# Optimization experiments

Measured on AMD Instinct MI355X. Metric: run time of the kernel, lower is better.

## Reference

```python
import jax, jax.numpy as jnp
import numpy as np

B_SZ, SEQ, D_MODEL = 2, 4096, 2048
EXPAND, D_STATE, D_CONV = 2, 16, 4
D_INNER = EXPAND * D_MODEL          # 4096
DT_RANK = -(-D_MODEL // 16)         # 128


def setup_inputs() -> dict:
    key = jax.random.key(0)
    ks = jax.random.split(key, 9)
    s = 0.02
    hidden_states = jax.random.normal(ks[0], (B_SZ, SEQ, D_MODEL), jnp.float32)
    W_in = jax.random.normal(ks[1], (2 * D_INNER, D_MODEL), jnp.float32) * s
    conv_w = jax.random.normal(ks[2], (D_INNER, D_CONV), jnp.float32) * 0.2
    conv_b = jnp.zeros((D_INNER,), jnp.float32)
    W_x = jax.random.normal(ks[3], (DT_RANK + 2 * D_STATE, D_INNER), jnp.float32) * s
    W_dt = jax.random.normal(ks[4], (D_INNER, DT_RANK), jnp.float32) * (DT_RANK ** -0.5)
    # dt bias so softplus(dt) ~ [1e-3, 0.1] as in Mamba init
    u = jax.random.uniform(ks[5], (D_INNER,), jnp.float32)
    dt = jnp.exp(u * (np.log(0.1) - np.log(1e-3)) + np.log(1e-3))
    dt_bias = dt + jnp.log(-jnp.expm1(-dt))  # inverse softplus
    # S4D-real init: A = -[1..d_state] per channel (kept negative for stability)
    A = -jnp.tile(jnp.arange(1.0, D_STATE + 1.0, dtype=jnp.float32), (D_INNER, 1))
    D = jnp.ones((D_INNER,), jnp.float32)
    W_out = jax.random.normal(ks[6], (D_MODEL, D_INNER), jnp.float32) * s
    return {"hidden_states": hidden_states, "W_in": W_in, "conv_w": conv_w,
            "conv_b": conv_b, "W_x": W_x, "W_dt": W_dt, "dt_bias": dt_bias,
            "A": A, "D": D, "W_out": W_out}


def _mamba_fwd(hidden_states, W_in, conv_w, conv_b, W_x, W_dt, dt_bias, A, D, W_out):
    # in_proj -> (B, L, 2*d_inner); split into x and gate z
    xz = jnp.einsum('bld,ed->ble', hidden_states, W_in)
    x, z = jnp.split(xz, 2, axis=-1)                    # (B,L,d_inner) each
    # causal depthwise conv1d over L (kernel d_conv), then SiLU
    d_conv = conv_w.shape[1]
    xp = jnp.pad(x, ((0, 0), (d_conv - 1, 0), (0, 0)))
    L = x.shape[1]
    xc = conv_b
    acc = jnp.zeros_like(x)
    for k in range(d_conv):                             # small fixed loop (4 taps)
        acc = acc + xp[:, k:k + L, :] * conv_w[:, k]
    x = jax.nn.silu(acc + conv_b)
    # x_proj -> dt_rank + 2*d_state
    ssm = jnp.einsum('bld,ed->ble', x, W_x)
    dt_r, Bm, Cm = jnp.split(ssm, [DT_RANK, DT_RANK + D_STATE], axis=-1)
    delta = jax.nn.softplus(jnp.einsum('blr,dr->bld', dt_r, W_dt) + dt_bias)
    # selective scan: h_t = exp(delta_t*A) h_{t-1} + delta_t*B_t*u_t ; y_t = C_t.h_t
    def step(state, inp):
        d_t, u_t, B_t, C_t = inp                        # (B,Di),(B,Di),(B,N),(B,N)
        dA = jnp.exp(d_t[..., None] * A)                # (B,Di,N)
        state = state * dA + (d_t * u_t)[..., None] * B_t[:, None, :]
        y = jnp.einsum('bdn,bn->bd', state, C_t)
        return state, y
    init = jnp.zeros((x.shape[0], D_INNER, D_STATE), jnp.float32)
    xs = (jnp.swapaxes(delta, 0, 1), jnp.swapaxes(x, 0, 1),
          jnp.swapaxes(Bm, 0, 1), jnp.swapaxes(Cm, 0, 1))
    _, ys = jax.lax.scan(step, init, xs)
    y = jnp.swapaxes(ys, 0, 1) + x * D                  # D skip connection
    y = y * jax.nn.silu(z)                              # gate
    return jnp.einsum('bld,md->blm', y, W_out)


def reference(hidden_states, W_in, conv_w, conv_b, W_x, W_dt, dt_bias, A, D, W_out):
    return _mamba_fwd(hidden_states, W_in, conv_w, conv_b, W_x, W_dt,
                      dt_bias, A, D, W_out)
```

## Files before the change

kernel.cpp:

```cpp
#include <hip/hip_runtime.h>
#include <hip/hip_bf16.h>
#include <cstdint>
#include <cstddef>

typedef _Float16 f16x8 __attribute__((ext_vector_type(8)));
typedef _Float16 f16x4 __attribute__((ext_vector_type(4)));
typedef float    f32x4 __attribute__((ext_vector_type(4)));

#define AS1 __attribute__((address_space(1)))
#define AS3 __attribute__((address_space(3)))

static constexpr int B_SZ = 2, SEQ = 4096, D_MODEL = 2048;
static constexpr int D_INNER = 4096, D_STATE = 16, D_CONV = 4, DT_RANK = 128;
static constexpr int M_ROWS = B_SZ * SEQ;
static constexpr int SSM_W  = DT_RANK + 2 * D_STATE;

__global__ __launch_bounds__(256) void k_cvt_f16(const float* __restrict__ in,
                                                 _Float16* __restrict__ out, int n4) {
    int i = blockIdx.x * 256 + threadIdx.x;
    if (i >= n4) return;
    f32x4 v = ((const f32x4*)in)[i];
    f16x4 h;
    h[0] = (_Float16)v[0]; h[1] = (_Float16)v[1];
    h[2] = (_Float16)v[2]; h[3] = (_Float16)v[3];
    ((f16x4*)out)[i] = h;
}

__global__ __launch_bounds__(256) void k_extract_dtr(const float* __restrict__ ssm,
                                                     _Float16* __restrict__ dtr) {
    int idx = blockIdx.x * 256 + threadIdx.x;
    if (idx >= M_ROWS * (DT_RANK / 4)) return;
    int m  = idx >> 5;
    int j4 = (idx & 31) * 4;
    f32x4 v = *(const f32x4*)&ssm[(size_t)m * SSM_W + j4];
    f16x4 h;
    h[0] = (_Float16)v[0]; h[1] = (_Float16)v[1];
    h[2] = (_Float16)v[2]; h[3] = (_Float16)v[3];
    *(f16x4*)&dtr[(size_t)m * DT_RANK + j4] = h;
}

template <int EPI>
__global__ __launch_bounds__(512, 2) void k_gemm256(
    const _Float16* __restrict__ A, const _Float16* __restrict__ Bm, int K, int nbx,
    void* __restrict__ out0, void* __restrict__ out1, int ldc) {
    __shared__ _Float16 lA[4][256][32];
    __shared__ _Float16 lB[4][256][32];

    const int tid  = threadIdx.x;
    const int l    = tid & 63;
    const int w    = tid >> 6;
    const int fr   = l & 15, fq = l >> 4;
    const int wrA  = (w >> 2) * 128;
    const int wcB  = (w & 3) * 64;

    const int nwg = gridDim.x;
    const int qq  = nwg >> 3;
    const int id  = (blockIdx.x & 7) * qq + (blockIdx.x >> 3);
    const int bx  = id % nbx, by = id / nbx;
    const int tileM = by * 256, tileN = bx * 256;

    const int srow = (l >> 2);
    const int cofs = (((l & 3) ^ ((l >> 2) & 3)) << 3);
    const int cswz = ((fq ^ (fr & 3)) << 3);

    f32x4 acc[8][4];
#pragma unroll
    for (int m = 0; m < 8; m++)
#pragma unroll
        for (int n = 0; n < 4; n++) acc[m][n] = (f32x4)0.f;

    const int NK = K >> 5;

    auto stage = [&](int ss, int kk) {
#pragma unroll
        for (int i = 0; i < 2; ++i) {
            const int u   = w * 2 + i;
            const int row = u * 16 + srow;
            const _Float16* ga = A  + (size_t)(tileM + row) * K + kk + cofs;
            const _Float16* gb = Bm + (size_t)(tileN + row) * K + kk + cofs;
            __builtin_amdgcn_global_load_lds((const AS1 void*)ga, (AS3 void*)&lA[ss][u * 16][0], 16, 0, 0);
            __builtin_amdgcn_global_load_lds((const AS1 void*)gb, (AS3 void*)&lB[ss][u * 16][0], 16, 0, 0);
        }
    };

    auto compute = [&](int ss) {
        f16x8 af[8], bf[4];
#pragma unroll
        for (int m = 0; m < 8; ++m)
            af[m] = *(const f16x8*)&lA[ss][wrA + m * 16 + fr][cswz];
#pragma unroll
        for (int n = 0; n < 4; ++n)
            bf[n] = *(const f16x8*)&lB[ss][wcB + n * 16 + fr][cswz];
        __builtin_amdgcn_s_setprio(1);
#pragma unroll
        for (int m = 0; m < 8; ++m)
#pragma unroll
            for (int n = 0; n < 4; ++n)
                acc[m][n] = __builtin_amdgcn_mfma_f32_16x16x32_f16(af[m], bf[n], acc[m][n], 0, 0, 0);
        __builtin_amdgcn_s_setprio(0);
    };

    stage(0, 0); stage(1, 32); stage(2, 64);
    asm volatile("s_waitcnt vmcnt(8)" ::: "memory");
    __builtin_amdgcn_s_barrier();

    for (int s = 0; s < NK - 3; ++s) {
        stage((s + 3) & 3, (s + 3) << 5);
        compute(s & 3);
        asm volatile("s_waitcnt vmcnt(8)" ::: "memory");
        __builtin_amdgcn_s_barrier();
    }
    compute((NK - 3) & 3);
    asm volatile("s_waitcnt vmcnt(4)" ::: "memory");
    __builtin_amdgcn_s_barrier();
    compute((NK - 2) & 3);
    asm volatile("s_waitcnt vmcnt(0)" ::: "memory");
    __builtin_amdgcn_s_barrier();
    compute((NK - 1) & 3);

#pragma unroll
    for (int m = 0; m < 8; ++m) {
#pragma unroll
        for (int n = 0; n < 4; ++n) {
            const int r0 = tileM + wrA + m * 16 + fq * 4;
            const int c  = tileN + wcB + n * 16 + fr;
#pragma unroll
            for (int q = 0; q < 4; ++q) {
                const float  v  = acc[m][n][q];
                const size_t mm = (size_t)(r0 + q);
                if (EPI == 0) {
                    if (c < D_INNER)
                        ((_Float16*)out0)[mm * D_INNER + c] = (_Float16)v;
                    else
                        ((_Float16*)out1)[mm * D_INNER + (c - D_INNER)] = (_Float16)v;
                } else {
                    ((float*)out0)[mm * ldc + c] = v;
                }
            }
        }
    }
}

template <int BM, int BN, int EPI>
__global__ __launch_bounds__(256) void k_gemm_nt(
    const _Float16* __restrict__ A, const _Float16* __restrict__ Bm, int K,
    int lda, int ldb, void* __restrict__ out0,
    const float* __restrict__ bias, int ldc) {
    __shared__ _Float16 a_lds[BM][32];
    __shared__ _Float16 b_lds[BN][32];
    constexpr int MR = BM / 32;
    constexpr int NR = BN / 32;
    const int tid  = threadIdx.x;
    const int lane = tid & 63;
    const int wid  = tid >> 6;
    const int wr = wid >> 1, wc = wid & 1;
    const int tileM = blockIdx.y * BM;
    const int tileN = blockIdx.x * BN;

    f32x4 acc[MR][NR];
    for (int i = 0; i < MR; i++)
        for (int j = 0; j < NR; j++) acc[i][j] = (f32x4)0.f;

    constexpr int IS_A = BM / 16;
    constexpr int IS_B = BN / 16;
    const int srow = lane >> 2;
    const int skof = (lane & 3) * 8;
    const int fr = lane & 15, fq = lane >> 4;

    for (int kk = 0; kk < K; kk += 32) {
        if (kk) __syncthreads();
        for (int is = wid; is < IS_A + IS_B; is += 4) {
            const bool isA = is < IS_A;
            const int  li  = isA ? is : is - IS_A;
            const int  row = li * 16 + srow;
            const _Float16* g =
                isA ? (A  + (size_t)(tileM + row) * lda + kk + skof)
                    : (Bm + (size_t)(tileN + row) * ldb + kk + skof);
            char* lp = ((char*)(isA ? &a_lds[0][0] : &b_lds[0][0])) + (size_t)li * 1024;
            __builtin_amdgcn_global_load_lds((const AS1 void*)g, (AS3 void*)lp, 16, 0, 0);
        }
        __syncthreads();

        f16x8 af[MR], bf[NR];
#pragma unroll
        for (int i = 0; i < MR; i++)
            af[i] = *(const f16x8*)&a_lds[wr * (BM / 2) + i * 16 + fr][fq * 8];
#pragma unroll
        for (int j = 0; j < NR; j++)
            bf[j] = *(const f16x8*)&b_lds[wc * (BN / 2) + j * 16 + fr][fq * 8];
#pragma unroll
        for (int i = 0; i < MR; i++)
#pragma unroll
            for (int j = 0; j < NR; j++)
                acc[i][j] = __builtin_amdgcn_mfma_f32_16x16x32_f16(af[i], bf[j], acc[i][j], 0, 0, 0);
    }

#pragma unroll
    for (int i = 0; i < MR; i++) {
#pragma unroll
        for (int j = 0; j < NR; j++) {
            const int r0 = tileM + wr * (BM / 2) + i * 16 + fq * 4;
            const int c  = tileN + wc * (BN / 2) + j * 16 + fr;
#pragma unroll
            for (int q = 0; q < 4; q++) {
                const float  v = acc[i][j][q];
                const size_t m = (size_t)(r0 + q);
                if (EPI == 1) {
                    ((float*)out0)[m * ldc + c] = v;
                } else {
                    float x  = v + bias[c];
                    float sp = (x > 20.f) ? x : log1pf(__expf(x));
                    ((_Float16*)out0)[m * ldc + c] = (_Float16)sp;
                }
            }
        }
    }
}

__global__ __launch_bounds__(256) void k_conv_silu(const _Float16* __restrict__ x,
                                                   const float* __restrict__ w,
                                                   const float* __restrict__ bias,
                                                   _Float16* __restrict__ out) {
    const int idx = blockIdx.x * 256 + threadIdx.x;
    const int d4 = idx & (D_INNER / 4 - 1);
    const int t  = (idx >> 10) & (SEQ - 1);
    const int b  = idx >> 22;
    const int d  = d4 * 4;
    const size_t rowbase = (size_t)b * SEQ * D_INNER;

    f32x4 wv[4];
#pragma unroll
    for (int i = 0; i < 4; i++) wv[i] = ((const f32x4*)w)[d + i];

    float acc[4];
#pragma unroll
    for (int i = 0; i < 4; i++) acc[i] = bias[d + i];
#pragma unroll
    for (int k = 0; k < D_CONV; k++) {
        int ti = t - (D_CONV - 1) + k;
        if (ti < 0) continue;
        f16x4 xv = *(const f16x4*)&x[rowbase + (size_t)ti * D_INNER + d];
#pragma unroll
        for (int i = 0; i < 4; i++) acc[i] += (float)xv[i] * wv[i][k];
    }
    f16x4 o;
#pragma unroll
    for (int i = 0; i < 4; i++) {
        float v = acc[i];
        o[i] = (_Float16)(v / (1.f + __expf(-v)));
    }
    *(f16x4*)&out[rowbase + (size_t)t * D_INNER + d] = o;
}

template <int CH, typename ST>
__global__ __launch_bounds__(256) void k_scan_p1(const _Float16* __restrict__ delta_h,
                                                 const _Float16* __restrict__ xc,
                                                 const float* __restrict__ ssm,
                                                 const float* __restrict__ Aptr,
                                                 ST* __restrict__ Sbuf,
                                                 ST* __restrict__ Pbuf) {
    constexpr int NCH = SEQ / CH;
    constexpr float L2E = 1.44269504088896f;
    const int bid   = blockIdx.x;
    const int dg    = bid & 15;
    const int chunk = (bid >> 4) % NCH;
    const int b     = bid / (16 * NCH);
    const int d     = dg * 256 + threadIdx.x;

    __shared__ float bsh[CH][D_STATE];
    const size_t rb = (size_t)b * SEQ + (size_t)chunk * CH;
    for (int i = threadIdx.x; i < CH * D_STATE; i += 256) {
        int t = i >> 4, n = i & 15;
        bsh[t][n] = ssm[(rb + t) * SSM_W + DT_RANK + n];
    }
    __syncthreads();

    float a2[D_STATE];
#pragma unroll
    for (int n = 0; n < D_STATE; n++) a2[n] = Aptr[(size_t)d * D_STATE + n] * L2E;
    float st[D_STATE];
#pragma unroll
    for (int n = 0; n < D_STATE; n++) st[n] = 0.f;
    float dtsum = 0.f;

    for (int t = 0; t < CH; ++t) {
        const size_t idx = (rb + t) * D_INNER + d;
        const float dt = (float)delta_h[idx];
        const float u  = (float)xc[idx];
        const float du = dt * u;
        dtsum += dt;
#pragma unroll
        for (int n = 0; n < D_STATE; n++) {
            float p = exp2f(dt * a2[n]);
            st[n] = st[n] * p + du * bsh[t][n];
        }
    }
    const size_t ob = ((size_t)(b * NCH + chunk) * D_STATE) * D_INNER + d;
#pragma unroll
    for (int n = 0; n < D_STATE; n++) {
        Sbuf[ob + (size_t)n * D_INNER] = (ST)st[n];
        Pbuf[ob + (size_t)n * D_INNER] = (ST)exp2f(dtsum * a2[n]);
    }
}

template <int NCH, typename ST>
__global__ __launch_bounds__(256) void k_scan_p2(ST* __restrict__ Sbuf,
                                                 const ST* __restrict__ Pbuf) {
    const int id = blockIdx.x * 256 + threadIdx.x;
    const int d = id & (D_INNER - 1);
    const int n = (id >> 12) & 15;
    const int b = id >> 16;
    float h = 0.f;
    for (int c = 0; c < NCH; ++c) {
        const size_t off = ((size_t)((b * NCH + c) * D_STATE + n)) * D_INNER + d;
        const float Pv = (float)Pbuf[off];
        const float Sv = (float)Sbuf[off];
        Sbuf[off] = (ST)h;
        h = Pv * h + Sv;
    }
}

template <int CH, typename ST>
__global__ __launch_bounds__(256) void k_scan_p3(const _Float16* __restrict__ delta_h,
                                                 const _Float16* __restrict__ xc,
                                                 const float* __restrict__ ssm,
                                                 const _Float16* __restrict__ z,
                                                 const float* __restrict__ Aptr,
                                                 const float* __restrict__ Dptr,
                                                 const ST* __restrict__ Sbuf,
                                                 _Float16* __restrict__ y_out) {
    constexpr int NCH = SEQ / CH;
    constexpr float L2E = 1.44269504088896f;
    const int bid   = blockIdx.x;
    const int dg    = bid & 15;
    const int chunk = (bid >> 4) % NCH;
    const int b     = bid / (16 * NCH);
    const int d     = dg * 256 + threadIdx.x;

    __shared__ float bsh[CH][2 * D_STATE];
    const size_t rb = (size_t)b * SEQ + (size_t)chunk * CH;
    for (int i = threadIdx.x; i < CH * 2 * D_STATE; i += 256) {
        int t = i >> 5, j = i & 31;
        bsh[t][j] = ssm[(rb + t) * SSM_W + DT_RANK + j];
    }
    __syncthreads();

    float a2[D_STATE];
#pragma unroll
    for (int n = 0; n < D_STATE; n++) a2[n] = Aptr[(size_t)d * D_STATE + n] * L2E;
    const float Dd = Dptr[d];

    const size_t ob = ((size_t)(b * NCH + chunk) * D_STATE) * D_INNER + d;
    float st[D_STATE];
#pragma unroll
    for (int n = 0; n < D_STATE; n++) st[n] = (float)Sbuf[ob + (size_t)n * D_INNER];

    for (int t = 0; t < CH; ++t) {
        const size_t idx = (rb + t) * D_INNER + d;
        const float dt = (float)delta_h[idx];
        const float u  = (float)xc[idx];
        const float du = dt * u;
        float y = 0.f;
#pragma unroll
        for (int n = 0; n < D_STATE; n++) {
            float p = exp2f(dt * a2[n]);
            st[n] = st[n] * p + du * bsh[t][n];
            y += st[n] * bsh[t][D_STATE + n];
        }
        const float zv = (float)z[idx];
        const float g  = zv / (1.f + __expf(-zv));
        y_out[idx] = (_Float16)((y + u * Dd) * g);
    }
}

__global__ __launch_bounds__(256) void k_scan(const _Float16* __restrict__ delta_h,
                                              const _Float16* __restrict__ xc,
                                              const float* __restrict__ ssm,
                                              const _Float16* __restrict__ z,
                                              const float* __restrict__ Aptr,
                                              const float* __restrict__ Dptr,
                                              _Float16* __restrict__ y_out) {
    const int b = blockIdx.x >> 4;
    const int d = (blockIdx.x & 15) * 256 + threadIdx.x;
    constexpr float L2E = 1.44269504088896f;
    float a2[D_STATE];
#pragma unroll
    for (int n = 0; n < D_STATE; n++) a2[n] = Aptr[(size_t)d * D_STATE + n] * L2E;
    const float Dd = Dptr[d];
    float st[D_STATE];
#pragma unroll
    for (int n = 0; n < D_STATE; n++) st[n] = 0.f;
    __shared__ float bc[128][32];
    const size_t rb = (size_t)b * SEQ;
    for (int tc = 0; tc < SEQ; tc += 128) {
        __syncthreads();
        for (int i = threadIdx.x; i < 128 * 32; i += 256) {
            int tl = i >> 5, j = i & 31;
            bc[tl][j] = ssm[(rb + tc + tl) * SSM_W + DT_RANK + j];
        }
        __syncthreads();
        for (int tl = 0; tl < 128; ++tl) {
            const size_t idx = (rb + tc + tl) * D_INNER + d;
            const float dt = (float)delta_h[idx];
            const float u  = (float)xc[idx];
            const float du = dt * u;
            float y = 0.f;
#pragma unroll
            for (int n = 0; n < D_STATE; n++) {
                float dA = exp2f(dt * a2[n]);
                st[n] = st[n] * dA + du * bc[tl][n];
                y += st[n] * bc[tl][D_STATE + n];
            }
            const float zv = (float)z[idx];
            const float g  = zv / (1.f + __expf(-zv));
            y_out[idx] = (_Float16)((y + u * Dd) * g);
        }
    }
}

template <int CH, typename ST>
static void launch_chunked_scan(const _Float16* delta_h, const _Float16* xc,
                                const float* ssm, const _Float16* z,
                                const float* Aptr, const float* Dptr,
                                ST* S, ST* P, _Float16* y, hipStream_t stream) {
    constexpr int NCH = SEQ / CH;
    k_scan_p1<CH, ST><<<B_SZ * NCH * 16, 256, 0, stream>>>(delta_h, xc, ssm, Aptr, S, P);
    k_scan_p2<NCH, ST><<<(B_SZ * 16 * D_INNER) / 256, 256, 0, stream>>>(S, P);
    k_scan_p3<CH, ST><<<B_SZ * NCH * 16, 256, 0, stream>>>(delta_h, xc, ssm, z, Aptr, Dptr, S, y);
}

extern "C" void kernel_launch(void* const* d_in, const int* in_sizes, int n_in,
                              void* d_out, int out_size, void* d_ws, size_t ws_size,
                              hipStream_t stream) {
    const float* hs    = (const float*)d_in[0];
    const float* W_in  = (const float*)d_in[1];
    const float* convw = (const float*)d_in[2];
    const float* convb = (const float*)d_in[3];
    const float* W_x   = (const float*)d_in[4];
    const float* W_dt  = (const float*)d_in[5];
    const float* dtb   = (const float*)d_in[6];
    const float* Aptr  = (const float*)d_in[7];
    const float* Dptr  = (const float*)d_in[8];
    const float* W_out = (const float*)d_in[9];

    char* ws = (char*)d_ws;
    _Float16* hs_h    = (_Float16*)(ws + 0);
    _Float16* Win_h   = (_Float16*)(ws + 33554432);
    _Float16* y_h     = (_Float16*)(ws + 0);
    _Float16* xraw    = (_Float16*)(ws + 67108864);
    _Float16* delta_h = (_Float16*)(ws + 67108864);
    _Float16* xc      = (_Float16*)(ws + 134217728);
    float*    ssm     = (float*)   (ws + 201326592);
    _Float16* dtr     = (_Float16*)(ws + 206569472);
    _Float16* Wx_h    = (_Float16*)(ws + 208666624);
    _Float16* Wdt_h   = (_Float16*)(ws + 209977344);
    _Float16* Wout_h  = (_Float16*)(ws + 211025920);
    _Float16* z_h     = (_Float16*)d_out;
    const size_t spbase = 227803136ull;

    auto cvt = [&](const float* in, _Float16* out, int n) {
        int n4 = n / 4;
        k_cvt_f16<<<(n4 + 255) / 256, 256, 0, stream>>>(in, out, n4);
    };
    cvt(hs,    hs_h,   B_SZ * SEQ * D_MODEL);
    cvt(W_in,  Win_h,  2 * D_INNER * D_MODEL);
    cvt(W_x,   Wx_h,   SSM_W * D_INNER);
    cvt(W_dt,  Wdt_h,  D_INNER * DT_RANK);
    cvt(W_out, Wout_h, D_MODEL * D_INNER);

    k_gemm256<0><<<(M_ROWS / 256) * (2 * D_INNER / 256), 512, 0, stream>>>(
        hs_h, Win_h, D_MODEL, 2 * D_INNER / 256, xraw, z_h, 0);

    k_conv_silu<<<(B_SZ * SEQ * (D_INNER / 4)) / 256, 256, 0, stream>>>(xraw, convw, convb, xc);

    k_gemm_nt<128, 32, 1><<<dim3(SSM_W / 32, M_ROWS / 128), 256, 0, stream>>>(
        xc, Wx_h, D_INNER, D_INNER, D_INNER, ssm, nullptr, SSM_W);

    k_extract_dtr<<<(M_ROWS * (DT_RANK / 4)) / 256, 256, 0, stream>>>(ssm, dtr);

    k_gemm_nt<128, 128, 2><<<dim3(D_INNER / 128, M_ROWS / 128), 256, 0, stream>>>(
        dtr, Wdt_h, DT_RANK, DT_RANK, DT_RANK, delta_h, dtb, D_INNER);

    {
        const size_t e64  = (size_t)B_SZ * (SEQ / 64)  * D_STATE * D_INNER;
        const size_t e128 = (size_t)B_SZ * (SEQ / 128) * D_STATE * D_INNER;
        if (ws_size >= spbase + 2 * e64 * sizeof(float)) {
            float* S = (float*)(ws + spbase);
            float* P = S + e64;
            launch_chunked_scan<64, float>(delta_h, xc, ssm, z_h, Aptr, Dptr, S, P, y_h, stream);
        } else if (ws_size >= spbase + 2 * e128 * sizeof(float)) {
            float* S = (float*)(ws + spbase);
            float* P = S + e128;
            launch_chunked_scan<128, float>(delta_h, xc, ssm, z_h, Aptr, Dptr, S, P, y_h, stream);
        } else if (ws_size >= spbase + 2 * e128 * sizeof(_Float16)) {
            _Float16* S = (_Float16*)(ws + spbase);
            _Float16* P = S + e128;
            launch_chunked_scan<128, _Float16>(delta_h, xc, ssm, z_h, Aptr, Dptr, S, P, y_h, stream);
        } else {
            k_scan<<<B_SZ * (D_INNER / 256), 256, 0, stream>>>(delta_h, xc, ssm, z_h, Aptr, Dptr, y_h);
        }
    }

    k_gemm256<1><<<(M_ROWS / 256) * (D_MODEL / 256), 512, 0, stream>>>(
        y_h, Wout_h, D_INNER, D_MODEL / 256, d_out, nullptr, D_MODEL);
}
```

Measured before the change: 1.271 ms.

## Restructure 256x256 GEMM into ping-pong K=64 double buffer with interleaved prefetch

Rewrites the large f16 MFMA GEMM used for in_proj and out_proj. It now uses two LDS buffers with K-tile 64 and an XOR swizzle over 8 chunks. Each K step is split into four MFMA quadrants, with LDS fragment loads and global prefetches interleaved between them under explicit barriers and setprio. Tile rasterization also changes so that consecutive ids walk along M instead of N. The aim is to hide global-to-LDS latency and LDS read stalls behind MFMA work, at the cost of many more barriers per iteration and a shallower prefetch depth.

```diff
diff --git a/kernel.cpp b/kernel.cpp
--- a/kernel.cpp
+++ b/kernel.cpp
@@ -40,28 +40,29 @@
 }
 
 template <int EPI>
-__global__ __launch_bounds__(512, 2) void k_gemm256(
-    const _Float16* __restrict__ A, const _Float16* __restrict__ Bm, int K, int nbx,
+__global__ __launch_bounds__(512, 2) void k_gemm256p(
+    const _Float16* __restrict__ A, const _Float16* __restrict__ Bm, int K, int nby,
     void* __restrict__ out0, void* __restrict__ out1, int ldc) {
-    __shared__ _Float16 lA[4][256][32];
-    __shared__ _Float16 lB[4][256][32];
-
-    const int tid  = threadIdx.x;
-    const int l    = tid & 63;
-    const int w    = tid >> 6;
-    const int fr   = l & 15, fq = l >> 4;
-    const int wrA  = (w >> 2) * 128;
-    const int wcB  = (w & 3) * 64;
-
-    const int nwg = gridDim.x;
-    const int qq  = nwg >> 3;
-    const int id  = (blockIdx.x & 7) * qq + (blockIdx.x >> 3);
-    const int bx  = id % nbx, by = id / nbx;
+    __shared__ _Float16 lA[2][256][64];
+    __shared__ _Float16 lB[2][256][64];
+    constexpr int LBUF = 256 * 64 * 2;
+
+    const int tid = threadIdx.x, l = tid & 63, w = tid >> 6;
+    const int fr = l & 15, fq = l >> 4;
+    const int wrA = (w >> 2) * 128;
+    const int wcB = (w & 3) * 64;
+
+    const int nwg = gridDim.x, qq = nwg >> 3;
+    const int id = (blockIdx.x & 7) * qq + (blockIdx.x >> 3);
+    const int by = id % nby, bx = id / nby;
     const int tileM = by * 256, tileN = bx * 256;
 
-    const int srow = (l >> 2);
-    const int cofs = (((l & 3) ^ ((l >> 2) & 3)) << 3);
-    const int cswz = ((fq ^ (fr & 3)) << 3);
+    const int rsub = l >> 3;
+    const int gco  = ((l & 7) ^ rsub) << 3;
+    const int swz0 = ((fq) ^ (fr & 7)) << 4;
+    const int swz1 = ((4 + fq) ^ (fr & 7)) << 4;
+
+    const int NK = K >> 6;
 
     f32x4 acc[8][4];
 #pragma unroll
@@ -69,54 +70,95 @@
 #pragma unroll
         for (int n = 0; n < 4; n++) acc[m][n] = (f32x4)0.f;
 
-    const int NK = K >> 5;
-
-    auto stage = [&](int ss, int kk) {
+    const char* cA = (const char*)lA;
+    const char* cB = (const char*)lB;
+
+    auto stageA = [&](int kt2, int h) {
 #pragma unroll
         for (int i = 0; i < 2; ++i) {
-            const int u   = w * 2 + i;
-            const int row = u * 16 + srow;
-            const _Float16* ga = A  + (size_t)(tileM + row) * K + kk + cofs;
-            const _Float16* gb = Bm + (size_t)(tileN + row) * K + kk + cofs;
-            __builtin_amdgcn_global_load_lds((const AS1 void*)ga, (AS3 void*)&lA[ss][u * 16][0], 16, 0, 0);
-            __builtin_amdgcn_global_load_lds((const AS1 void*)gb, (AS3 void*)&lB[ss][u * 16][0], 16, 0, 0);
+            const int brow = h * 128 + (w * 2 + i) * 8;
+            const _Float16* g = A + (size_t)(tileM + brow + rsub) * K + kt2 * 64 + gco;
+            __builtin_amdgcn_global_load_lds((const AS1 void*)g,
+                (AS3 void*)&lA[kt2 & 1][brow][0], 16, 0, 0);
         }
     };
-
-    auto compute = [&](int ss) {
-        f16x8 af[8], bf[4];
-#pragma unroll
-        for (int m = 0; m < 8; ++m)
-            af[m] = *(const f16x8*)&lA[ss][wrA + m * 16 + fr][cswz];
-#pragma unroll
-        for (int n = 0; n < 4; ++n)
-            bf[n] = *(const f16x8*)&lB[ss][wcB + n * 16 + fr][cswz];
-        __builtin_amdgcn_s_setprio(1);
-#pragma unroll
-        for (int m = 0; m < 8; ++m)
-#pragma unroll
-            for (int n = 0; n < 4; ++n)
-                acc[m][n] = __builtin_amdgcn_mfma_f32_16x16x32_f16(af[m], bf[n], acc[m][n], 0, 0, 0);
-        __builtin_amdgcn_s_setprio(0);
+    auto stageB = [&](int kt2, int h) {
+#pragma unroll
+        for (int i = 0; i < 2; ++i) {
+            const int brow = h * 128 + (w * 2 + i) * 8;
+            const _Float16* g = Bm + (size_t)(tileN + brow + rsub) * K + kt2 * 64 + gco;
+            __builtin_amdgcn_global_load_lds((const AS1 void*)g,
+                (AS3 void*)&lB[kt2 & 1][brow][0], 16, 0, 0);
+        }
     };
 
-    stage(0, 0); stage(1, 32); stage(2, 64);
+#pragma unroll
+    for (int t = 0; t < 2; ++t) {
+        stageA(t, 0); stageA(t, 1); stageB(t, 0); stageB(t, 1);
+    }
     asm volatile("s_waitcnt vmcnt(8)" ::: "memory");
     __builtin_amdgcn_s_barrier();
 
-    for (int s = 0; s < NK - 3; ++s) {
-        stage((s + 3) & 3, (s + 3) << 5);
-        compute(s & 3);
-        asm volatile("s_waitcnt vmcnt(8)" ::: "memory");
-        __builtin_amdgcn_s_barrier();
-    }
-    compute((NK - 3) & 3);
-    asm volatile("s_waitcnt vmcnt(4)" ::: "memory");
-    __builtin_amdgcn_s_barrier();
-    compute((NK - 2) & 3);
-    asm volatile("s_waitcnt vmcnt(0)" ::: "memory");
-    __builtin_amdgcn_s_barrier();
-    compute((NK - 1) & 3);
+    f16x8 af[4][2], bf0[2][2], bf1[2][2];
+
+#define MFMA_QUAD(MO, NO, BF)                                                        \
+    __builtin_amdgcn_s_setprio(1);                                                   \
+    _Pragma("unroll") for (int m = 0; m < 4; ++m)                                    \
+    _Pragma("unroll") for (int n = 0; n < 2; ++n)                                    \
+    _Pragma("unroll") for (int kk = 0; kk < 2; ++kk)                                 \
+        acc[(MO) + m][(NO) + n] = __builtin_amdgcn_mfma_f32_16x16x32_f16(            \
+            af[m][kk], BF[n][kk], acc[(MO) + m][(NO) + n], 0, 0, 0);                 \
+    __builtin_amdgcn_s_setprio(0);
+
+    for (int kt = 0; kt < NK; ++kt) {
+        const int buf = kt & 1;
+        const bool pf = (kt + 2 < NK);
+#pragma unroll
+        for (int m = 0; m < 4; ++m) {
+            af[m][0] = *(const f16x8*)(cA + buf * LBUF + (wrA + m * 16 + fr) * 128 + swz0);
+            af[m][1] = *(const f16x8*)(cA + buf * LBUF + (wrA + m * 16 + fr) * 128 + swz1);
+        }
+#pragma unroll
+        for (int n = 0; n < 2; ++n) {
+            bf0[n][0] = *(const f16x8*)(cB + buf * LBUF + (wcB + n * 16 + fr) * 128 + swz0);
+            bf0[n][1] = *(const f16x8*)(cB + buf * LBUF + (wcB + n * 16 + fr) * 128 + swz1);
+        }
+        __builtin_amdgcn_s_barrier();
+        asm volatile("s_waitcnt lgkmcnt(0)" ::: "memory");
+        __builtin_amdgcn_sched_barrier(0);
+        MFMA_QUAD(0, 0, bf0)
+        __builtin_amdgcn_s_barrier();
+#pragma unroll
+        for (int n = 0; n < 2; ++n) {
+            bf1[n][0] = *(const f16x8*)(cB + buf * LBUF + (wcB + (n + 2) * 16 + fr) * 128 + swz0);
+            bf1[n][1] = *(const f16x8*)(cB + buf * LBUF + (wcB + (n + 2) * 16 + fr) * 128 + swz1);
+        }
+        __builtin_amdgcn_s_barrier();
+        asm volatile("s_waitcnt lgkmcnt(0)" ::: "memory");
+        __builtin_amdgcn_sched_barrier(0);
+        MFMA_QUAD(0, 2, bf1)
+        __builtin_amdgcn_s_barrier();
+#pragma unroll
+        for (int m = 0; m < 4; ++m) {
+            af[m][0] = *(const f16x8*)(cA + buf * LBUF + (wrA + (m + 4) * 16 + fr) * 128 + swz0);
+            af[m][1] = *(const f16x8*)(cA + buf * LBUF + (wrA + (m + 4) * 16 + fr) * 128 + swz1);
+        }
+        if (pf) { stageB(kt + 2, 0); stageB(kt + 2, 1); }
+        __builtin_amdgcn_s_barrier();
+        asm volatile("s_waitcnt lgkmcnt(0)" ::: "memory");
+        __builtin_amdgcn_sched_barrier(0);
+        MFMA_QUAD(4, 0, bf0)
+        __builtin_amdgcn_s_barrier();
+        if (pf) { stageA(kt + 2, 0); stageA(kt + 2, 1); }
+        __builtin_amdgcn_s_barrier();
+        MFMA_QUAD(4, 2, bf1)
+        if (kt < NK - 1) {
+            if (pf) { asm volatile("s_waitcnt vmcnt(8)" ::: "memory"); }
+            else    { asm volatile("s_waitcnt vmcnt(0)" ::: "memory"); }
+            __builtin_amdgcn_s_barrier();
+        }
+    }
+#undef MFMA_QUAD
 
 #pragma unroll
     for (int m = 0; m < 8; ++m) {
@@ -468,8 +510,8 @@
     cvt(W_dt,  Wdt_h,  D_INNER * DT_RANK);
     cvt(W_out, Wout_h, D_MODEL * D_INNER);
 
-    k_gemm256<0><<<(M_ROWS / 256) * (2 * D_INNER / 256), 512, 0, stream>>>(
-        hs_h, Win_h, D_MODEL, 2 * D_INNER / 256, xraw, z_h, 0);
+    k_gemm256p<0><<<(M_ROWS / 256) * (2 * D_INNER / 256), 512, 0, stream>>>(
+        hs_h, Win_h, D_MODEL, M_ROWS / 256, xraw, z_h, 0);
 
     k_conv_silu<<<(B_SZ * SEQ * (D_INNER / 4)) / 256, 256, 0, stream>>>(xraw, convw, convb, xc);
 
@@ -501,6 +543,6 @@
         }
     }
 
-    k_gemm256<1><<<(M_ROWS / 256) * (D_MODEL / 256), 512, 0, stream>>>(
-        y_h, Wout_h, D_INNER, D_MODEL / 256, d_out, nullptr, D_MODEL);
-}
+    k_gemm256p<1><<<(M_ROWS / 256) * (D_MODEL / 256), 512, 0, stream>>>(
+        y_h, Wout_h, D_INNER, M_ROWS / 256, d_out, nullptr, D_MODEL);
+}
```

Result: faster. 1.138 ms (-10.5%).
